# Performance work log

Measured on AMD Instinct MI355X. Metric: run time of the kernel, lower is better.

Reference implementation:

```python
import jax, jax.numpy as jnp
import numpy as np

VOCAB = 32000


def setup_inputs() -> dict:
    key = jax.random.key(0)
    k1, k2, k3, k4, k5 = jax.random.split(key, 5)
    B, H, DEC_T, ATTN_LEN, D = 16, 12, 128, 512, 768
    return {
        "dec_output": jax.random.normal(k1, (B, DEC_T, D), dtype=jnp.float32),
        "final_output": jax.random.normal(k2, (B, DEC_T, VOCAB), dtype=jnp.float32),
        "attention_weights": jax.random.normal(k3, (B, H, DEC_T, ATTN_LEN), dtype=jnp.float32),
        "encoder_input": jax.random.randint(k4, (B, ATTN_LEN), 0, VOCAB, dtype=jnp.int32),
        "W_pg": jax.random.normal(k5, (D, 1), dtype=jnp.float32) / np.sqrt(D),
        "b_pg": jnp.zeros((1,), dtype=jnp.float32),
    }


def reference(dec_output, final_output, attention_weights, encoder_input, W_pg, b_pg):
    # p_gen: Dense(1) + sigmoid  -> [B, dec_t, 1]
    p_gen = jax.nn.sigmoid(dec_output @ W_pg + b_pg)

    vocab_dist = jax.nn.softmax(final_output, axis=-1)          # [B, dec_t, V]

    # mean_attention_heads=True: average over the heads axis
    attn_mean = jnp.mean(attention_weights, axis=1)              # [B, dec_t, attn_len]
    attn_dist = jax.nn.softmax(attn_mean, axis=-1)

    vocab_dists = p_gen * vocab_dist
    attn_dists = (1.0 - p_gen) * attn_dist

    dec_t = attn_dist.shape[1]

    # Per-example scatter-add of attention mass onto vocab ids.
    # For each batch b: proj[t, encoder_input[b, j]] += attn_dists[b, t, j]
    def scatter_one(ids, a):  # ids: [attn_len] int, a: [dec_t, attn_len]
        return jnp.zeros((dec_t, VOCAB), dtype=a.dtype).at[:, ids].add(a)

    attn_dists_projected = jax.vmap(scatter_one)(encoder_input, attn_dists)

    final_dists = attn_dists_projected + vocab_dists
    return jnp.log(final_dists)
```

## Files before the change

kernel.cpp:

```cpp
#include <hip/hip_runtime.h>
#include <math.h>

#define VOCAB 32000
#define NB 16
#define NH 12
#define DEC_T 128
#define ALEN 512
#define DD 768
#define NT 512
#define NW 8
#define V4 8000
#define CHUNKS 16
#define HSZ 1024
#define HMASK (HSZ - 1)
#define BMW (VOCAB / 32)
#define HEMPTY 0xFFFFFFFFu

__device__ inline float wave_sum(float v) {
#pragma unroll
  for (int o = 32; o > 0; o >>= 1) v += __shfl_down(v, o, 64);
  return v;
}
__device__ inline float wave_max(float v) {
#pragma unroll
  for (int o = 32; o > 0; o >>= 1) v = fmaxf(v, __shfl_down(v, o, 64));
  return v;
}

__global__ __launch_bounds__(NT, 4) void pg_kernel(
    const float* __restrict__ dec, const float* __restrict__ fo,
    const float* __restrict__ attnw, const int* __restrict__ ids,
    const float* __restrict__ Wpg, const float* __restrict__ bpg,
    float* __restrict__ out) {
  __shared__ unsigned s_bm[BMW];
  __shared__ unsigned s_key[HSZ];
  __shared__ float    s_val[HSZ];
  __shared__ float    s_red[NW];
  __shared__ float    s_res[8];

  const int bt = blockIdx.x;
  const int b = bt / DEC_T;
  const int t = bt - b * DEC_T;
  const int tid = threadIdx.x;
  const int lane = tid & 63;
  const int wid = tid >> 6;

  const float4* row4 = (const float4*)(fo + (size_t)bt * VOCAB);
  float4 r[CHUNKS];
#pragma unroll
  for (int c = 0; c < CHUNKS; ++c) {
    int idx = c * NT + tid;
    if (idx < V4) r[c] = row4[idx];
  }

  for (int i = tid; i < BMW; i += NT) s_bm[i] = 0u;
  for (int i = tid; i < HSZ; i += NT) { s_key[i] = HEMPTY; s_val[i] = 0.f; }

  float pp = dec[(size_t)bt * DD + tid] * Wpg[tid];
  if (tid < DD - NT) pp += dec[(size_t)bt * DD + NT + tid] * Wpg[NT + tid];
  pp = wave_sum(pp);
  if (lane == 0) s_red[wid] = pp;
  __syncthreads();
  if (tid == 0) {
    float a = 0.f;
    for (int i = 0; i < NW; ++i) a += s_red[i];
    s_res[0] = a;
  }
  __syncthreads();
  const float pgen = 1.f / (1.f + __expf(-(s_res[0] + bpg[0])));

  const float* ap = attnw + ((size_t)b * NH * DEC_T + t) * ALEN + tid;
  float s = 0.f;
#pragma unroll
  for (int h = 0; h < NH; ++h) s += ap[(size_t)h * DEC_T * ALEN];
  const float amean = s * (1.f / NH);
  float am = wave_max(amean);
  if (lane == 0) s_red[wid] = am;
  __syncthreads();
  if (tid == 0) {
    float a = -INFINITY;
    for (int i = 0; i < NW; ++i) a = fmaxf(a, s_red[i]);
    s_res[1] = a;
  }
  __syncthreads();
  const float ae = __expf(amean - s_res[1]);
  float as = wave_sum(ae);
  if (lane == 0) s_red[wid] = as;
  __syncthreads();
  if (tid == 0) {
    float a = 0.f;
    for (int i = 0; i < NW; ++i) a += s_red[i];
    s_res[2] = a;
  }
  __syncthreads();
  const float ainv = (1.f - pgen) / s_res[2];

  {
    const float w = ae * ainv;
    const unsigned id = (unsigned)ids[b * ALEN + tid];
    atomicOr(&s_bm[id >> 5], 1u << (id & 31));
    unsigned h = (id * 2654435761u) >> 22;
    for (;;) {
      unsigned old = atomicCAS(&s_key[h], HEMPTY, id);
      if (old == HEMPTY || old == id) { atomicAdd(&s_val[h], w); break; }
      h = (h + 1) & HMASK;
    }
  }

  float m = -INFINITY;
#pragma unroll
  for (int c = 0; c < CHUNKS; ++c) {
    int idx = c * NT + tid;
    if (idx < V4)
      m = fmaxf(m, fmaxf(fmaxf(r[c].x, r[c].y), fmaxf(r[c].z, r[c].w)));
  }
  m = wave_max(m);
  if (lane == 0) s_red[wid] = m;
  __syncthreads();
  if (tid == 0) {
    float a = -INFINITY;
    for (int i = 0; i < NW; ++i) a = fmaxf(a, s_red[i]);
    s_res[3] = a;
  }
  __syncthreads();
  const float fm = s_res[3];

  float zs = 0.f;
#pragma unroll
  for (int c = 0; c < CHUNKS; ++c) {
    int idx = c * NT + tid;
    if (idx < V4)
      zs += __expf(r[c].x - fm) + __expf(r[c].y - fm) +
            __expf(r[c].z - fm) + __expf(r[c].w - fm);
  }
  zs = wave_sum(zs);
  if (lane == 0) s_red[wid] = zs;
  __syncthreads();
  if (tid == 0) {
    float a = 0.f;
    for (int i = 0; i < NW; ++i) a += s_red[i];
    s_res[4] = a;
  }
  __syncthreads();
  const float Z = s_res[4];
  const float invZ = 1.f / Z;
  const float C = __logf(pgen) - fm - __logf(Z);

  auto hget = [&](unsigned id) -> float {
    unsigned h = (id * 2654435761u) >> 22;
    while (s_key[h] != id) h = (h + 1) & HMASK;
    return s_val[h];
  };

  float4* out4 = (float4*)(out + (size_t)bt * VOCAB);
#pragma unroll
  for (int c = 0; c < CHUNKS; ++c) {
    int idx = c * NT + tid;
    if (idx < V4) {
      const float4 x = r[c];
      float4 o;
      const unsigned nib = (s_bm[idx >> 3] >> ((idx & 7) * 4)) & 0xFu;
      if (nib == 0u) {
        o.x = x.x + C; o.y = x.y + C; o.z = x.z + C; o.w = x.w + C;
      } else {
        const unsigned v = (unsigned)idx * 4u;
        o.x = (nib & 1u) ? __logf(pgen * __expf(x.x - fm) * invZ + hget(v + 0u)) : (x.x + C);
        o.y = (nib & 2u) ? __logf(pgen * __expf(x.y - fm) * invZ + hget(v + 1u)) : (x.y + C);
        o.z = (nib & 4u) ? __logf(pgen * __expf(x.z - fm) * invZ + hget(v + 2u)) : (x.z + C);
        o.w = (nib & 8u) ? __logf(pgen * __expf(x.w - fm) * invZ + hget(v + 3u)) : (x.w + C);
      }
      out4[idx] = o;
    }
  }
}

extern "C" void kernel_launch(void* const* d_in, const int* in_sizes, int n_in,
                              void* d_out, int out_size, void* d_ws, size_t ws_size,
                              hipStream_t stream) {
  (void)in_sizes; (void)n_in; (void)out_size; (void)d_ws; (void)ws_size;
  const float* dec   = (const float*)d_in[0];
  const float* fo    = (const float*)d_in[1];
  const float* attnw = (const float*)d_in[2];
  const int*   ids   = (const int*)  d_in[3];
  const float* Wpg   = (const float*)d_in[4];
  const float* bpg   = (const float*)d_in[5];
  float* out = (float*)d_out;

  pg_kernel<<<NB * DEC_T, NT, 0, stream>>>(dec, fo, attnw, ids, Wpg, bpg, out);
}
```

Baseline: 509.2 us.

## Merge block reductions into fewer barriers and hoist small loads early

Replaces the serial tid==0 reductions, each followed by an extra barrier, with separate shared arrays that every thread reduces redundantly. The reductions are interleaved so only three barriers remain instead of ten. Scatter weights are stored unnormalized and scaled by the attention normalizer at lookup time. The attention, dec and ids loads are issued before the big row load to overlap latency. The cost is redundant per-thread reduction reads of shared memory and extra registers held across the vocab row load.

```diff
diff --git a/kernel.cpp b/kernel.cpp
--- a/kernel.cpp
+++ b/kernel.cpp
@@ -35,8 +35,11 @@
   __shared__ unsigned s_bm[BMW];
   __shared__ unsigned s_key[HSZ];
   __shared__ float    s_val[HSZ];
-  __shared__ float    s_red[NW];
-  __shared__ float    s_res[8];
+  __shared__ float    s_redA[NW];
+  __shared__ float    s_redB[NW];
+  __shared__ float    s_redC[NW];
+  __shared__ float    s_redD[NW];
+  __shared__ float    s_redE[NW];
 
   const int bt = blockIdx.x;
   const int b = bt / DEC_T;
@@ -44,6 +47,14 @@
   const int tid = threadIdx.x;
   const int lane = tid & 63;
   const int wid = tid >> 6;
+
+  const float* ap = attnw + ((size_t)b * NH * DEC_T + t) * ALEN + tid;
+  float hsum = 0.f;
+#pragma unroll
+  for (int h = 0; h < NH; ++h) hsum += ap[(size_t)h * DEC_T * ALEN];
+  float pp = dec[(size_t)bt * DD + tid] * Wpg[tid];
+  if (tid < DD - NT) pp += dec[(size_t)bt * DD + NT + tid] * Wpg[NT + tid];
+  const unsigned myid = (unsigned)ids[b * ALEN + tid];
 
   const float4* row4 = (const float4*)(fo + (size_t)bt * VOCAB);
   float4 r[CHUNKS];
@@ -56,53 +67,30 @@
   for (int i = tid; i < BMW; i += NT) s_bm[i] = 0u;
   for (int i = tid; i < HSZ; i += NT) { s_key[i] = HEMPTY; s_val[i] = 0.f; }
 
-  float pp = dec[(size_t)bt * DD + tid] * Wpg[tid];
-  if (tid < DD - NT) pp += dec[(size_t)bt * DD + NT + tid] * Wpg[NT + tid];
+  const float amean = hsum * (1.f / NH);
+  float am = wave_max(amean);
+  if (lane == 0) s_redA[wid] = am;
   pp = wave_sum(pp);
-  if (lane == 0) s_red[wid] = pp;
+  if (lane == 0) s_redB[wid] = pp;
   __syncthreads();
-  if (tid == 0) {
-    float a = 0.f;
-    for (int i = 0; i < NW; ++i) a += s_red[i];
-    s_res[0] = a;
+
+  float amax = -INFINITY, pdot = 0.f;
+#pragma unroll
+  for (int i = 0; i < NW; ++i) {
+    amax = fmaxf(amax, s_redA[i]);
+    pdot += s_redB[i];
   }
-  __syncthreads();
-  const float pgen = 1.f / (1.f + __expf(-(s_res[0] + bpg[0])));
+  const float pgen = 1.f / (1.f + __expf(-(pdot + bpg[0])));
+  const float ae = __expf(amean - amax);
+  float as = wave_sum(ae);
+  if (lane == 0) s_redC[wid] = as;
 
-  const float* ap = attnw + ((size_t)b * NH * DEC_T + t) * ALEN + tid;
-  float s = 0.f;
-#pragma unroll
-  for (int h = 0; h < NH; ++h) s += ap[(size_t)h * DEC_T * ALEN];
-  const float amean = s * (1.f / NH);
-  float am = wave_max(amean);
-  if (lane == 0) s_red[wid] = am;
-  __syncthreads();
-  if (tid == 0) {
-    float a = -INFINITY;
-    for (int i = 0; i < NW; ++i) a = fmaxf(a, s_red[i]);
-    s_res[1] = a;
-  }
-  __syncthreads();
-  const float ae = __expf(amean - s_res[1]);
-  float as = wave_sum(ae);
-  if (lane == 0) s_red[wid] = as;
-  __syncthreads();
-  if (tid == 0) {
-    float a = 0.f;
-    for (int i = 0; i < NW; ++i) a += s_red[i];
-    s_res[2] = a;
-  }
-  __syncthreads();
-  const float ainv = (1.f - pgen) / s_res[2];
-
+  atomicOr(&s_bm[myid >> 5], 1u << (myid & 31));
   {
-    const float w = ae * ainv;
-    const unsigned id = (unsigned)ids[b * ALEN + tid];
-    atomicOr(&s_bm[id >> 5], 1u << (id & 31));
-    unsigned h = (id * 2654435761u) >> 22;
+    unsigned h = (myid * 2654435761u) >> 22;
     for (;;) {
-      unsigned old = atomicCAS(&s_key[h], HEMPTY, id);
-      if (old == HEMPTY || old == id) { atomicAdd(&s_val[h], w); break; }
+      unsigned old = atomicCAS(&s_key[h], HEMPTY, myid);
+      if (old == HEMPTY || old == myid) { atomicAdd(&s_val[h], ae); break; }
       h = (h + 1) & HMASK;
     }
   }
@@ -115,16 +103,16 @@
       m = fmaxf(m, fmaxf(fmaxf(r[c].x, r[c].y), fmaxf(r[c].z, r[c].w)));
   }
   m = wave_max(m);
-  if (lane == 0) s_red[wid] = m;
+  if (lane == 0) s_redD[wid] = m;
   __syncthreads();
-  if (tid == 0) {
-    float a = -INFINITY;
-    for (int i = 0; i < NW; ++i) a = fmaxf(a, s_red[i]);
-    s_res[3] = a;
+
+  float asum = 0.f, fm = -INFINITY;
+#pragma unroll
+  for (int i = 0; i < NW; ++i) {
+    asum += s_redC[i];
+    fm = fmaxf(fm, s_redD[i]);
   }
-  __syncthreads();
-  const float fm = s_res[3];
-
+  const float ainv = (1.f - pgen) / asum;
   float zs = 0.f;
 #pragma unroll
   for (int c = 0; c < CHUNKS; ++c) {
@@ -134,15 +122,12 @@
             __expf(r[c].z - fm) + __expf(r[c].w - fm);
   }
   zs = wave_sum(zs);
-  if (lane == 0) s_red[wid] = zs;
+  if (lane == 0) s_redE[wid] = zs;
   __syncthreads();
-  if (tid == 0) {
-    float a = 0.f;
-    for (int i = 0; i < NW; ++i) a += s_red[i];
-    s_res[4] = a;
-  }
-  __syncthreads();
-  const float Z = s_res[4];
+
+  float Z = 0.f;
+#pragma unroll
+  for (int i = 0; i < NW; ++i) Z += s_redE[i];
   const float invZ = 1.f / Z;
   const float C = __logf(pgen) - fm - __logf(Z);
 
@@ -164,10 +149,10 @@
         o.x = x.x + C; o.y = x.y + C; o.z = x.z + C; o.w = x.w + C;
       } else {
         const unsigned v = (unsigned)idx * 4u;
-        o.x = (nib & 1u) ? __logf(pgen * __expf(x.x - fm) * invZ + hget(v + 0u)) : (x.x + C);
-        o.y = (nib & 2u) ? __logf(pgen * __expf(x.y - fm) * invZ + hget(v + 1u)) : (x.y + C);
-        o.z = (nib & 4u) ? __logf(pgen * __expf(x.z - fm) * invZ + hget(v + 2u)) : (x.z + C);
-        o.w = (nib & 8u) ? __logf(pgen * __expf(x.w - fm) * invZ + hget(v + 3u)) : (x.w + C);
+        o.x = (nib & 1u) ? __logf(pgen * __expf(x.x - fm) * invZ + hget(v + 0u) * ainv) : (x.x + C);
+        o.y = (nib & 2u) ? __logf(pgen * __expf(x.y - fm) * invZ + hget(v + 1u) * ainv) : (x.y + C);
+        o.z = (nib & 4u) ? __logf(pgen * __expf(x.z - fm) * invZ + hget(v + 2u) * ainv) : (x.z + C);
+        o.w = (nib & 8u) ? __logf(pgen * __expf(x.w - fm) * invZ + hget(v + 3u) * ainv) : (x.w + C);
       }
       out4[idx] = o;
     }
```

Result: no change. 513.1 us (+0.8%).
